# Kernel optimization log

Measured on AMD Instinct MI355X. Metric: run time of the kernel, lower is better.

## Reference

```python
import jax, jax.numpy as jnp
import numpy as np

N_E = 8192
E_DIM = 64
BETA = 0.25


def setup_inputs() -> dict:
    key = jax.random.key(0)
    k_z, k_e = jax.random.split(key)
    z = jax.random.normal(k_z, (16, E_DIM, 64, 64), dtype=jnp.float32)  # b c h w
    # nn.Embedding weight init: uniform(-1/n_e, 1/n_e)
    embedding = jax.random.uniform(
        k_e, (N_E, E_DIM), dtype=jnp.float32, minval=-1.0 / N_E, maxval=1.0 / N_E
    )
    return {"z": z, "embedding": embedding}


def reference(z, embedding):
    # b c h w -> b h w c
    zc = jnp.transpose(z, (0, 2, 3, 1))
    zf = zc.reshape(-1, embedding.shape[1])  # [N, d]
    # squared euclidean distances: ||z||^2 + ||e||^2 - 2 z.e
    d = (
        jnp.sum(zf * zf, axis=1, keepdims=True)
        + jnp.sum(embedding * embedding, axis=1)
        - 2.0 * jnp.einsum("nd,kd->nk", zf, embedding)
    )  # [N, K]
    min_encoding_indices = jnp.argmin(d, axis=1)  # [N]
    z_q = jnp.take(embedding, min_encoding_indices, axis=0).reshape(zc.shape)
    # legacy=True loss
    loss = jnp.mean((jax.lax.stop_gradient(z_q) - zc) ** 2) + BETA * jnp.mean(
        (z_q - jax.lax.stop_gradient(zc)) ** 2
    )
    # straight-through estimator
    z_q = zc + jax.lax.stop_gradient(z_q - zc)
    z_q = jnp.transpose(z_q, (0, 3, 1, 2))  # b h w c -> b c h w
    return z_q, loss, min_encoding_indices
```

## Files before the change

### kernel.cpp

```cpp
#include <hip/hip_runtime.h>

#define NTOT 65536
#define KC   8192
#define DV   64
#define ZQN  4194304
#define NSPL 4
#define KSL  2048
#define TILE 128
#define NTILE 16
#define CAP2 16
#define SLA  44u
#define SLE  40u

typedef unsigned int u32;
typedef unsigned long long u64;
typedef unsigned short ushort;
typedef short short8 __attribute__((ext_vector_type(8)));
typedef float float4v __attribute__((ext_vector_type(4)));

__device__ __forceinline__ short f2bf(float x) {
    u32 u = __float_as_uint(x);
    u32 r = (u + 0x7fffu + ((u >> 16) & 1u)) >> 16;
    return (short)r;
}

__device__ __forceinline__ float exact_d(float A, float B,
                                         const float* __restrict__ zr,
                                         const float* __restrict__ e) {
#pragma clang fp contract(off)
    float u0 = 0.f, u1 = 0.f, u2 = 0.f, u3 = 0.f;
#pragma unroll
    for (int i = 0; i < 4; ++i) {
        const int t = 16 * i;
        u0 = (zr[t+0]*e[t+0]) + ((zr[t+4]*e[t+4]) + ((zr[t+8]*e[t+8]) + ((zr[t+12]*e[t+12]) + u0)));
        u1 = (zr[t+1]*e[t+1]) + ((zr[t+5]*e[t+5]) + ((zr[t+9]*e[t+9]) + ((zr[t+13]*e[t+13]) + u1)));
        u2 = (zr[t+2]*e[t+2]) + ((zr[t+6]*e[t+6]) + ((zr[t+10]*e[t+10]) + ((zr[t+14]*e[t+14]) + u2)));
        u3 = (zr[t+3]*e[t+3]) + ((zr[t+7]*e[t+7]) + ((zr[t+11]*e[t+11]) + ((zr[t+15]*e[t+15]) + u3)));
    }
    float dot = (u0 + u1) + (u2 + u3);
    return (A + B) - (2.0f * dot);
}

__global__ __launch_bounds__(256) void vq_prep(
    const float* __restrict__ emb, float* __restrict__ nrm,
    u32* __restrict__ cnt, double* __restrict__ lacc,
    u32* __restrict__ oflowCnt, ushort* __restrict__ ebs) {
    const int tid = blockIdx.x * 256 + threadIdx.x;
    const int t = tid >> 10, r = tid & 1023;
    const int s = r >> 7, r2 = r & 127, h = r2 >> 6, l = r2 & 63;
    const int q = l >> 4, c = l & 15;
    const float* src = emb + (size_t)((t * 128 + s * 16 + c) * 64 + h * 32 + q * 8);
    short8 v;
#pragma unroll
    for (int j = 0; j < 8; ++j) v[j] = f2bf(src[j]);
    *reinterpret_cast<short8*>(ebs + (size_t)tid * 8) = v;
    cnt[tid] = 0u;
    if (tid < KC) {
        double sacc = 0.0;
#pragma unroll
        for (int d = 0; d < DV; ++d) {
            double x = (double)emb[(size_t)tid * DV + d];
            sacc = fma(x, x, sacc);
        }
        nrm[tid] = (float)sacc;
    }
    if (tid == 0) { *lacc = 0.0; *oflowCnt = 0u; }
}

__global__ __launch_bounds__(256) __attribute__((amdgpu_waves_per_eu(4, 4)))
void vq_pass(const float* __restrict__ z, const ushort* __restrict__ ebs,
             u32* __restrict__ cnt, u32* __restrict__ cand) {
    __shared__ ushort tileS[TILE * DV];
    const int tid = threadIdx.x;
    const int lane = tid & 63;
    const int nblk = blockIdx.x & 255, ks = blockIdx.x >> 8;
    const int nb = nblk * 256 + (tid >> 6) * 64;
    const int col = lane & 15, quad = lane >> 4;
    const int nlo = nb + col;

    short8 zf[4][2];
#pragma unroll
    for (int ns = 0; ns < 4; ++ns) {
        int n = nlo + ns * 16;
        const float* zp = z + (size_t)(n >> 12) * 262144 + (n & 4095);
#pragma unroll
        for (int t2 = 0; t2 < 2; ++t2)
#pragma unroll
            for (int j = 0; j < 8; ++j)
                zf[ns][t2][j] = f2bf(zp[(size_t)(t2 * 32 + quad * 8 + j) * 4096]);
    }

    u32 r0[4] = {0, 0, 0, 0}, r1[4] = {0, 0, 0, 0}, r2[4] = {0, 0, 0, 0};
    const char* gs = (const char*)ebs + (size_t)ks * (KSL * DV * 2);

    int4 pre[4];
#pragma unroll
    for (int j = 0; j < 4; ++j)
        pre[j] = *reinterpret_cast<const int4*>(gs + j * 4096 + tid * 16);

    for (int t = 0; t < NTILE; ++t) {
        __syncthreads();
#pragma unroll
        for (int j = 0; j < 4; ++j)
            *reinterpret_cast<int4*>((char*)tileS + j * 4096 + tid * 16) = pre[j];
        __syncthreads();
        if (t < NTILE - 1) {
#pragma unroll
            for (int j = 0; j < 4; ++j)
                pre[j] = *reinterpret_cast<const int4*>(
                    gs + (size_t)(t + 1) * 16384 + j * 4096 + tid * 16);
        }
#pragma unroll
        for (int g2 = 0; g2 < 4; ++g2) {
            const char* tb = (const char*)tileS + g2 * 4096;
            short8 a00 = *reinterpret_cast<const short8*>(tb + lane * 16);
            short8 a01 = *reinterpret_cast<const short8*>(tb + 1024 + lane * 16);
            short8 a10 = *reinterpret_cast<const short8*>(tb + 2048 + lane * 16);
            short8 a11 = *reinterpret_cast<const short8*>(tb + 3072 + lane * 16);
            const u32 lowc = 0x80000000u + (u32)(((t * 4 + g2) << 2) | quad);
#pragma unroll
            for (int ns = 0; ns < 4; ++ns) {
                float4v acc0 = {0.f, 0.f, 0.f, 0.f};
                float4v acc1 = {0.f, 0.f, 0.f, 0.f};
                acc0 = __builtin_amdgcn_mfma_f32_16x16x32_bf16(a00, zf[ns][0], acc0, 0, 0, 0);
                acc0 = __builtin_amdgcn_mfma_f32_16x16x32_bf16(a01, zf[ns][1], acc0, 0, 0, 0);
                acc1 = __builtin_amdgcn_mfma_f32_16x16x32_bf16(a10, zf[ns][0], acc1, 0, 0, 0);
                acc1 = __builtin_amdgcn_mfma_f32_16x16x32_bf16(a11, zf[ns][1], acc1, 0, 0, 0);
                float m = fmaxf(fmaxf(fmaxf(acc0[0], acc0[1]), fmaxf(acc0[2], acc0[3])),
                                fmaxf(fmaxf(acc1[0], acc1[1]), fmaxf(acc1[2], acc1[3])));
                u32 e = ((u32)(int)(m * 1048576.0f) << 16) + lowc;
                u32 x  = min(r0[ns], e);
                r0[ns] = max(r0[ns], e);
                u32 y  = min(r1[ns], x);
                r1[ns] = max(r1[ns], x);
                r2[ns] = max(r2[ns], y);
            }
        }
    }

#pragma unroll
    for (int ns = 0; ns < 4; ++ns) {
        u32 m = r0[ns];
        m = max(m, __shfl_xor(m, 16));
        m = max(m, __shfl_xor(m, 32));
        const u32 thr = (m & 0xffff0000u) - (SLA << 16);
        const int n = nlo + ns * 16;
        const u32 tag = (u32)ks << 8;
        if (r0[ns] >= thr) {
            u32 p = atomicAdd(&cnt[n], 1u);
            if (p < CAP2) cand[(size_t)n * CAP2 + p] = r0[ns] | tag;
        }
        if (r1[ns] >= thr) {
            u32 p = atomicAdd(&cnt[n], 1u);
            if (p < CAP2) cand[(size_t)n * CAP2 + p] = r1[ns] | tag;
        }
        if (r2[ns] >= thr) {
            u32 p = atomicAdd(&cnt[n], 1u);
            if (p < CAP2) cand[(size_t)n * CAP2 + p] = r2[ns] | tag;
        }
    }
}

__global__ __launch_bounds__(256) void vq_e1(
    const float* __restrict__ z, const float* __restrict__ emb,
    const float* __restrict__ nrm, const u32* __restrict__ cnt,
    const u32* __restrict__ cand, int* __restrict__ idxw,
    float* __restrict__ out, u32* __restrict__ oflowCnt,
    int* __restrict__ oflowList) {
    const int gid = blockIdx.x * 256 + threadIdx.x;
    const int n = gid >> 2, j4 = gid & 3;
    u32 c = cnt[n];
    if (c > CAP2) {
        if (j4 == 0) {
            u32 p = atomicAdd(oflowCnt, 1u);
            oflowList[p] = n;
            idxw[n] = 0;
            out[(size_t)ZQN + 1 + n] = 0.f;
        }
        return;
    }
    u32 emax = 0u;
    for (u32 j = 0; j < c; ++j) {
        u32 e = cand[(size_t)n * CAP2 + j];
        if (e > emax) emax = e;
    }
    const u32 ethr = (emax & 0xffff0000u) - (SLE << 16);

    const float* zp = z + (size_t)(n >> 12) * 262144 + (n & 4095);
    float zr[DV];
#pragma unroll
    for (int d = 0; d < DV; ++d) zr[d] = zp[(size_t)d * 4096];
    double ad = 0.0;
#pragma unroll
    for (int d = 0; d < DV; ++d) ad = fma((double)zr[d], (double)zr[d], ad);
    const float A = (float)ad;

    float dmin = 1e30f;
    int kmin = 0x7fffffff;
    for (u32 j = (u32)j4; j < c; j += 4) {
        u32 e = cand[(size_t)n * CAP2 + j];
        if (e < ethr) continue;
        int s   = (int)(e >> 8) & 3;
        int grp = (int)(e >> 2) & 63;
        int q   = (int)e & 3;
        int base = s * KSL + grp * 32 + q * 4;
#pragma unroll
        for (int st = 0; st < 2; ++st)
#pragma unroll
            for (int r = 0; r < 4; ++r) {
                int k = base + st * 16 + r;
                float d = exact_d(A, nrm[k], zr, emb + (size_t)k * DV);
                if (d < dmin || (d == dmin && k < kmin)) { dmin = d; kmin = k; }
            }
    }
    u64 key = ((u64)__float_as_uint(dmin) << 32) | (u32)kmin;
    u64 o1 = __shfl_xor(key, 1, 64); if (o1 < key) key = o1;
    u64 o2 = __shfl_xor(key, 2, 64); if (o2 < key) key = o2;
    if (j4 == 0) {
        int km = (int)(key & 0xffffffffu);
        idxw[n] = km;
        out[(size_t)ZQN + 1 + n] = (float)km;
    }
}

__global__ __launch_bounds__(256) void vq_e1b(
    const float* __restrict__ z, const float* __restrict__ emb,
    const float* __restrict__ nrm, const u32* __restrict__ oflowCnt,
    const int* __restrict__ oflowList, int* __restrict__ idxw,
    float* __restrict__ out) {
    __shared__ u64 red[4];
    const int tid = threadIdx.x;
    const int nof = (int)*oflowCnt;
    for (int i = blockIdx.x; i < nof; i += gridDim.x) {
        const int n = oflowList[i];
        const float* zp = z + (size_t)(n >> 12) * 262144 + (n & 4095);
        float zr[DV];
#pragma unroll
        for (int d = 0; d < DV; ++d) zr[d] = zp[(size_t)d * 4096];
        double ad = 0.0;
#pragma unroll
        for (int d = 0; d < DV; ++d) ad = fma((double)zr[d], (double)zr[d], ad);
        const float A = (float)ad;
        u64 best = ~0ull;
        for (int k = tid; k < KC; k += 256) {
            float d = exact_d(A, nrm[k], zr, emb + (size_t)k * DV);
            u64 key = ((u64)__float_as_uint(d) << 32) | (u32)k;
            if (key < best) best = key;
        }
#pragma unroll
        for (int off = 32; off > 0; off >>= 1) {
            u64 o = __shfl_down(best, off, 64);
            if (o < best) best = o;
        }
        if ((tid & 63) == 0) red[tid >> 6] = best;
        __syncthreads();
        if (tid == 0) {
            u64 b = red[0];
#pragma unroll
            for (int w = 1; w < 4; ++w) if (red[w] < b) b = red[w];
            int kmin = (int)(b & 0xffffffffu);
            idxw[n] = kmin;
            out[(size_t)ZQN + 1 + n] = (float)kmin;
        }
        __syncthreads();
    }
}

__global__ __launch_bounds__(256) void vq_e2(
    const float* __restrict__ z, const float* __restrict__ emb,
    const int* __restrict__ idxw, float* __restrict__ out,
    double* __restrict__ lacc) {
    __shared__ double red[4];
    const int tid = threadIdx.x;
    const int n = blockIdx.x * 64 + (tid & 63);
    const int part = tid >> 6;
    const int b = n >> 12, hw = n & 4095;
    const int kmin = idxw[n];
    const float* zp = z + (size_t)b * 262144 + hw;
    const float4* er4 = (const float4*)(emb + (size_t)kmin * DV + part * 16);
    double lsum = 0.0;
#pragma unroll
    for (int i4 = 0; i4 < 4; ++i4) {
        float4 ev = er4[i4];
#pragma unroll
        for (int u = 0; u < 4; ++u) {
            int c = part * 16 + i4 * 4 + u;
            float v = (u == 0) ? ev.x : (u == 1) ? ev.y : (u == 2) ? ev.z : ev.w;
            out[(size_t)b * 262144 + (size_t)c * 4096 + hw] = v;
            double dv = (double)v - (double)zp[(size_t)c * 4096];
            lsum = fma(dv, dv, lsum);
        }
    }
#pragma unroll
    for (int off = 32; off > 0; off >>= 1)
        lsum += __shfl_down(lsum, off, 64);
    if ((tid & 63) == 0) red[tid >> 6] = lsum;
    __syncthreads();
    if (tid == 0)
        atomicAdd(lacc, red[0] + red[1] + red[2] + red[3]);
}

__global__ void vq_fin(const double* __restrict__ lacc, float* __restrict__ out) {
    if (threadIdx.x == 0)
        out[ZQN] = (float)(1.25 * (*lacc) / (double)ZQN);
}

extern "C" void kernel_launch(void* const* d_in, const int* in_sizes, int n_in,
                              void* d_out, int out_size, void* d_ws, size_t ws_size,
                              hipStream_t stream) {
    const float* z   = (const float*)d_in[0];
    const float* emb = (const float*)d_in[1];
    float* out = (float*)d_out;

    ushort* ebs  = (ushort*)d_out;
    u32*    cand = (u32*)((char*)d_out + 1048576);
    double* lacc  = (double*)d_ws;
    u32*    oflowCnt = (u32*)((char*)d_ws + 8);
    float*  nrm   = (float*)((char*)d_ws + 64);
    u32*    cnt   = (u32*)((char*)d_ws + 32832);
    int*    idxw  = (int*)((char*)d_ws + 294976);
    int*    oflowList = (int*)((char*)d_ws + 557120);

    vq_prep<<<256, 256, 0, stream>>>(emb, nrm, cnt, lacc, oflowCnt, ebs);
    vq_pass<<<NSPL * 256, 256, 0, stream>>>(z, ebs, cnt, cand);
    vq_e1<<<1024, 256, 0, stream>>>(z, emb, nrm, cnt, cand, idxw, out,
                                    oflowCnt, oflowList);
    vq_e1b<<<128, 256, 0, stream>>>(z, emb, nrm, oflowCnt, oflowList, idxw, out);
    vq_e2<<<1024, 256, 0, stream>>>(z, emb, idxw, out, lacc);
    vq_fin<<<1, 64, 0, stream>>>(lacc, out);
}
```

Before: 253.9 us.

## Coarsen candidate groups to 16 codes and split exact rescoring across 8 lanes

The approximate pass now merges the max over two consecutive 8-code groups before updating the top-3 candidate registers. This halves the packing and sorting-network work per MFMA result. Each candidate therefore covers 16 codewords instead of 8. To absorb that, the exact rescoring kernel assigns 8 threads per row, each half-pair taking two of the four 4-code strips, and launches twice as many blocks. The cost is coarser candidate filtering and therefore more exact distance evaluations, plus the z row being reloaded by twice as many threads.

```diff
diff --git a/kernel.cpp b/kernel.cpp
--- a/kernel.cpp
+++ b/kernel.cpp
@@ -91,6 +91,7 @@
     }
 
     u32 r0[4] = {0, 0, 0, 0}, r1[4] = {0, 0, 0, 0}, r2[4] = {0, 0, 0, 0};
+    float mprev[4];
     const char* gs = (const char*)ebs + (size_t)ks * (KSL * DV * 2);
 
     int4 pre[4];
@@ -117,7 +118,8 @@
             short8 a01 = *reinterpret_cast<const short8*>(tb + 1024 + lane * 16);
             short8 a10 = *reinterpret_cast<const short8*>(tb + 2048 + lane * 16);
             short8 a11 = *reinterpret_cast<const short8*>(tb + 3072 + lane * 16);
-            const u32 lowc = 0x80000000u + (u32)(((t * 4 + g2) << 2) | quad);
+            const u32 lowc = 0x80000000u +
+                             (u32)((((t * 2) + (g2 >> 1)) << 2) | quad);
 #pragma unroll
             for (int ns = 0; ns < 4; ++ns) {
                 float4v acc0 = {0.f, 0.f, 0.f, 0.f};
@@ -126,14 +128,20 @@
                 acc0 = __builtin_amdgcn_mfma_f32_16x16x32_bf16(a01, zf[ns][1], acc0, 0, 0, 0);
                 acc1 = __builtin_amdgcn_mfma_f32_16x16x32_bf16(a10, zf[ns][0], acc1, 0, 0, 0);
                 acc1 = __builtin_amdgcn_mfma_f32_16x16x32_bf16(a11, zf[ns][1], acc1, 0, 0, 0);
-                float m = fmaxf(fmaxf(fmaxf(acc0[0], acc0[1]), fmaxf(acc0[2], acc0[3])),
-                                fmaxf(fmaxf(acc1[0], acc1[1]), fmaxf(acc1[2], acc1[3])));
-                u32 e = ((u32)(int)(m * 1048576.0f) << 16) + lowc;
-                u32 x  = min(r0[ns], e);
-                r0[ns] = max(r0[ns], e);
-                u32 y  = min(r1[ns], x);
-                r1[ns] = max(r1[ns], x);
-                r2[ns] = max(r2[ns], y);
+                float q0 = fmaxf(fmaxf(acc0[0], acc0[1]), acc0[2]);
+                float q1 = fmaxf(fmaxf(acc0[3], acc1[0]), acc1[1]);
+                float q2 = fmaxf(fmaxf(acc1[2], acc1[3]), q0);
+                if ((g2 & 1) == 0) {
+                    mprev[ns] = fmaxf(q2, q1);
+                } else {
+                    float m = fmaxf(fmaxf(q2, q1), mprev[ns]);
+                    u32 e = ((u32)(int)(m * 1048576.0f) << 16) + lowc;
+                    u32 x  = min(r0[ns], e);
+                    r0[ns] = max(r0[ns], e);
+                    u32 y  = min(r1[ns], x);
+                    r1[ns] = max(r1[ns], x);
+                    r2[ns] = max(r2[ns], y);
+                }
             }
         }
     }
@@ -168,10 +176,10 @@
     float* __restrict__ out, u32* __restrict__ oflowCnt,
     int* __restrict__ oflowList) {
     const int gid = blockIdx.x * 256 + threadIdx.x;
-    const int n = gid >> 2, j4 = gid & 3;
+    const int n = gid >> 3, j8 = gid & 7;
     u32 c = cnt[n];
     if (c > CAP2) {
-        if (j4 == 0) {
+        if (j8 == 0) {
             u32 p = atomicAdd(oflowCnt, 1u);
             oflowList[p] = n;
             idxw[n] = 0;
@@ -197,18 +205,20 @@
 
     float dmin = 1e30f;
     int kmin = 0x7fffffff;
-    for (u32 j = (u32)j4; j < c; j += 4) {
+    const int st0 = (j8 & 1) * 2;
+    for (u32 j = (u32)(j8 >> 1); j < c; j += 4) {
         u32 e = cand[(size_t)n * CAP2 + j];
         if (e < ethr) continue;
-        int s   = (int)(e >> 8) & 3;
-        int grp = (int)(e >> 2) & 63;
-        int q   = (int)e & 3;
-        int base = s * KSL + grp * 32 + q * 4;
+        int s    = (int)(e >> 8) & 3;
+        int cell = (int)e & 0x7f;
+        int grp  = cell >> 2;
+        int q    = cell & 3;
+        int base = s * KSL + grp * 64 + q * 4;
 #pragma unroll
         for (int st = 0; st < 2; ++st)
 #pragma unroll
             for (int r = 0; r < 4; ++r) {
-                int k = base + st * 16 + r;
+                int k = base + (st0 + st) * 16 + r;
                 float d = exact_d(A, nrm[k], zr, emb + (size_t)k * DV);
                 if (d < dmin || (d == dmin && k < kmin)) { dmin = d; kmin = k; }
             }
@@ -216,7 +226,8 @@
     u64 key = ((u64)__float_as_uint(dmin) << 32) | (u32)kmin;
     u64 o1 = __shfl_xor(key, 1, 64); if (o1 < key) key = o1;
     u64 o2 = __shfl_xor(key, 2, 64); if (o2 < key) key = o2;
-    if (j4 == 0) {
+    u64 o4 = __shfl_xor(key, 4, 64); if (o4 < key) key = o4;
+    if (j8 == 0) {
         int km = (int)(key & 0xffffffffu);
         idxw[n] = km;
         out[(size_t)ZQN + 1 + n] = (float)km;
@@ -323,7 +334,7 @@
 
     vq_prep<<<256, 256, 0, stream>>>(emb, nrm, cnt, lacc, oflowCnt, ebs);
     vq_pass<<<NSPL * 256, 256, 0, stream>>>(z, ebs, cnt, cand);
-    vq_e1<<<1024, 256, 0, stream>>>(z, emb, nrm, cnt, cand, idxw, out,
+    vq_e1<<<2048, 256, 0, stream>>>(z, emb, nrm, cnt, cand, idxw, out,
                                     oflowCnt, oflowList);
     vq_e1b<<<128, 256, 0, stream>>>(z, emb, nrm, oflowCnt, oflowList, idxw, out);
     vq_e2<<<1024, 256, 0, stream>>>(z, emb, idxw, out, lacc);
```

Result: slower. 284.1 us (+11.9%).

## Precompute row norms in prep and widen candidate rescoring to 8 lanes per row

Applied to the files above, without the earlier changes.

Computes the squared norm of each z row once in the prep kernel and stores it in workspace, so the rescoring kernel no longer recomputes it. The rescoring kernel now stages a 32-row z tile through shared memory with vectorized loads and splits each candidate's two 4-code halves across lanes, so each row uses 8 lanes and the grid doubles. The max reduction in the main pass is reassociated into a different tree. Prep kernel takes on strided z reads, and the extra shuffle step plus shared staging add overhead.

```diff
diff --git a/kernel.cpp b/kernel.cpp
--- a/kernel.cpp
+++ b/kernel.cpp
@@ -42,7 +42,8 @@
 }
 
 __global__ __launch_bounds__(256) void vq_prep(
-    const float* __restrict__ emb, float* __restrict__ nrm,
+    const float* __restrict__ emb, const float* __restrict__ z,
+    float* __restrict__ nrm, float* __restrict__ An,
     u32* __restrict__ cnt, double* __restrict__ lacc,
     u32* __restrict__ oflowCnt, ushort* __restrict__ ebs) {
     const int tid = blockIdx.x * 256 + threadIdx.x;
@@ -55,6 +56,16 @@
     for (int j = 0; j < 8; ++j) v[j] = f2bf(src[j]);
     *reinterpret_cast<short8*>(ebs + (size_t)tid * 8) = v;
     cnt[tid] = 0u;
+    {
+        const float* zp = z + (size_t)(tid >> 12) * 262144 + (tid & 4095);
+        double ad = 0.0;
+#pragma unroll
+        for (int d = 0; d < DV; ++d) {
+            double x = (double)zp[(size_t)d * 4096];
+            ad = fma(x, x, ad);
+        }
+        An[tid] = (float)ad;
+    }
     if (tid < KC) {
         double sacc = 0.0;
 #pragma unroll
@@ -126,8 +137,10 @@
                 acc0 = __builtin_amdgcn_mfma_f32_16x16x32_bf16(a01, zf[ns][1], acc0, 0, 0, 0);
                 acc1 = __builtin_amdgcn_mfma_f32_16x16x32_bf16(a10, zf[ns][0], acc1, 0, 0, 0);
                 acc1 = __builtin_amdgcn_mfma_f32_16x16x32_bf16(a11, zf[ns][1], acc1, 0, 0, 0);
-                float m = fmaxf(fmaxf(fmaxf(acc0[0], acc0[1]), fmaxf(acc0[2], acc0[3])),
-                                fmaxf(fmaxf(acc1[0], acc1[1]), fmaxf(acc1[2], acc1[3])));
+                float q0 = fmaxf(fmaxf(acc0[0], acc0[1]), acc0[2]);
+                float q1 = fmaxf(fmaxf(acc0[3], acc1[0]), acc1[1]);
+                float q2 = fmaxf(fmaxf(acc1[2], acc1[3]), q0);
+                float m  = fmaxf(q2, q1);
                 u32 e = ((u32)(int)(m * 1048576.0f) << 16) + lowc;
                 u32 x  = min(r0[ns], e);
                 r0[ns] = max(r0[ns], e);
@@ -163,15 +176,32 @@
 
 __global__ __launch_bounds__(256) void vq_e1(
     const float* __restrict__ z, const float* __restrict__ emb,
-    const float* __restrict__ nrm, const u32* __restrict__ cnt,
-    const u32* __restrict__ cand, int* __restrict__ idxw,
-    float* __restrict__ out, u32* __restrict__ oflowCnt,
-    int* __restrict__ oflowList) {
-    const int gid = blockIdx.x * 256 + threadIdx.x;
-    const int n = gid >> 2, j4 = gid & 3;
+    const float* __restrict__ nrm, const float* __restrict__ An,
+    const u32* __restrict__ cnt, const u32* __restrict__ cand,
+    int* __restrict__ idxw, float* __restrict__ out,
+    u32* __restrict__ oflowCnt, int* __restrict__ oflowList) {
+    __shared__ float zs[64][40];
+    const int tid = threadIdx.x;
+    const int n0 = blockIdx.x * 32;
+    const int b = n0 >> 12, hw0 = n0 & 4095;
+    {
+        const float* zb = z + (size_t)b * 262144 + hw0;
+        const int dS = tid >> 3, i4 = (tid & 7) * 4;
+#pragma unroll
+        for (int j = 0; j < 2; ++j) {
+            const int d = dS + 32 * j;
+            float4 v = *reinterpret_cast<const float4*>(zb + (size_t)d * 4096 + i4);
+            *reinterpret_cast<float4*>(&zs[d][i4]) = v;
+        }
+    }
+    __syncthreads();
+
+    const int li = tid >> 3;
+    const int n = n0 + li;
+    const int j8 = tid & 7;
     u32 c = cnt[n];
     if (c > CAP2) {
-        if (j4 == 0) {
+        if (j8 == 0) {
             u32 p = atomicAdd(oflowCnt, 1u);
             oflowList[p] = n;
             idxw[n] = 0;
@@ -186,37 +216,33 @@
     }
     const u32 ethr = (emax & 0xffff0000u) - (SLE << 16);
 
-    const float* zp = z + (size_t)(n >> 12) * 262144 + (n & 4095);
     float zr[DV];
 #pragma unroll
-    for (int d = 0; d < DV; ++d) zr[d] = zp[(size_t)d * 4096];
-    double ad = 0.0;
-#pragma unroll
-    for (int d = 0; d < DV; ++d) ad = fma((double)zr[d], (double)zr[d], ad);
-    const float A = (float)ad;
+    for (int d = 0; d < DV; ++d) zr[d] = zs[d][li];
+    const float A = An[n];
 
     float dmin = 1e30f;
     int kmin = 0x7fffffff;
-    for (u32 j = (u32)j4; j < c; j += 4) {
+    const int st = j8 & 1;
+    for (u32 j = (u32)(j8 >> 1); j < c; j += 4) {
         u32 e = cand[(size_t)n * CAP2 + j];
         if (e < ethr) continue;
         int s   = (int)(e >> 8) & 3;
         int grp = (int)(e >> 2) & 63;
         int q   = (int)e & 3;
-        int base = s * KSL + grp * 32 + q * 4;
-#pragma unroll
-        for (int st = 0; st < 2; ++st)
-#pragma unroll
-            for (int r = 0; r < 4; ++r) {
-                int k = base + st * 16 + r;
-                float d = exact_d(A, nrm[k], zr, emb + (size_t)k * DV);
-                if (d < dmin || (d == dmin && k < kmin)) { dmin = d; kmin = k; }
-            }
+        int base = s * KSL + grp * 32 + q * 4 + st * 16;
+#pragma unroll
+        for (int r = 0; r < 4; ++r) {
+            int k = base + r;
+            float d = exact_d(A, nrm[k], zr, emb + (size_t)k * DV);
+            if (d < dmin || (d == dmin && k < kmin)) { dmin = d; kmin = k; }
+        }
     }
     u64 key = ((u64)__float_as_uint(dmin) << 32) | (u32)kmin;
     u64 o1 = __shfl_xor(key, 1, 64); if (o1 < key) key = o1;
     u64 o2 = __shfl_xor(key, 2, 64); if (o2 < key) key = o2;
-    if (j4 == 0) {
+    u64 o4 = __shfl_xor(key, 4, 64); if (o4 < key) key = o4;
+    if (j8 == 0) {
         int km = (int)(key & 0xffffffffu);
         idxw[n] = km;
         out[(size_t)ZQN + 1 + n] = (float)km;
@@ -320,10 +346,11 @@
     u32*    cnt   = (u32*)((char*)d_ws + 32832);
     int*    idxw  = (int*)((char*)d_ws + 294976);
     int*    oflowList = (int*)((char*)d_ws + 557120);
-
-    vq_prep<<<256, 256, 0, stream>>>(emb, nrm, cnt, lacc, oflowCnt, ebs);
+    float*  An    = (float*)((char*)d_ws + 819264);
+
+    vq_prep<<<256, 256, 0, stream>>>(emb, z, nrm, An, cnt, lacc, oflowCnt, ebs);
     vq_pass<<<NSPL * 256, 256, 0, stream>>>(z, ebs, cnt, cand);
-    vq_e1<<<1024, 256, 0, stream>>>(z, emb, nrm, cnt, cand, idxw, out,
+    vq_e1<<<2048, 256, 0, stream>>>(z, emb, nrm, An, cnt, cand, idxw, out,
                                     oflowCnt, oflowList);
     vq_e1b<<<128, 256, 0, stream>>>(z, emb, nrm, oflowCnt, oflowList, idxw, out);
     vq_e2<<<1024, 256, 0, stream>>>(z, emb, idxw, out, lacc);
```

After: 235.4 us. 7.3% less time.
